# Optimization experiments

Hardware: AMD Instinct MI355X
Metric: run time of the kernel (lower is better)

The kernel has to match this reference:

```python
import jax, jax.numpy as jnp
import numpy as np

N_NODES = 50000
N_EDGES = 1500000
D = 512
LN_EPS = 1e-5


def setup_inputs() -> dict:
    key = jax.random.key(0)
    ks = jax.random.split(key, 8)
    scale = 1.0 / np.sqrt(D)
    return {
        "node_feature": jax.random.normal(ks[0], (N_NODES, D), dtype=jnp.float32),
        "edge_index": jax.random.randint(ks[1], (2, N_EDGES), 0, N_NODES, dtype=jnp.int32),
        "W_l": jax.random.uniform(ks[2], (D, D), jnp.float32, -scale, scale),  # neighbor lin
        "b_l": jnp.zeros((D,), jnp.float32),
        "W_r": jax.random.uniform(ks[3], (D, D), jnp.float32, -scale, scale),  # root lin (no bias)
        "gamma": jnp.ones((D,), jnp.float32),
        "beta": jnp.zeros((D,), jnp.float32),
    }


def _layer_norm(x, gamma, beta):
    mu = jnp.mean(x, axis=-1, keepdims=True)
    var = jnp.mean(jnp.square(x - mu), axis=-1, keepdims=True)
    return (x - mu) * jax.lax.rsqrt(var + LN_EPS) * gamma + beta


def reference(node_feature, edge_index, W_l, b_l, W_r, gamma, beta):
    n = node_feature.shape[0]
    residual = node_feature
    h = _layer_norm(node_feature, gamma, beta)
    src, dst = edge_index[0], edge_index[1]
    # mean-aggregate source features at destinations (gather + segment scatter)
    summed = jax.ops.segment_sum(h[src], dst, num_segments=n)  # [N, D]
    cnt = jax.ops.segment_sum(jnp.ones((src.shape[0],), h.dtype), dst, num_segments=n)
    mean = summed / jnp.maximum(cnt, 1.0)[:, None]
    # SAGEConv: lin_l(aggregated) + lin_r(root); bias on lin_l
    out = mean @ W_l.T + b_l + h @ W_r.T
    out = jax.nn.relu(out)
    return out + residual
```

## Files before the change

kernel.cpp:

```cpp
#include <hip/hip_runtime.h>


#define D_DIM 512

typedef __bf16 bf16x8 __attribute__((ext_vector_type(8)));
typedef float f32x4 __attribute__((ext_vector_type(4)));
typedef float f32x2 __attribute__((ext_vector_type(2)));

__device__ __forceinline__ unsigned short f2bf(float f) {
  unsigned u = __float_as_uint(f);
  u += 0x7fffu + ((u >> 16) & 1u);
  return (unsigned short)(u >> 16);
}
__device__ __forceinline__ float bflo(unsigned u) { return __uint_as_float(u << 16); }
__device__ __forceinline__ float bfhi(unsigned u) { return __uint_as_float(u & 0xffff0000u); }
__device__ __forceinline__ unsigned packbf2(float lo, float hi) {
  return (unsigned)f2bf(lo) | ((unsigned)f2bf(hi) << 16);
}

__global__ void ln_kernel(const float* __restrict__ x, const float* __restrict__ gamma,
                          const float* __restrict__ beta, unsigned short* __restrict__ Acat,
                          unsigned char* __restrict__ h8, int n, int use_fp8) {
  int lane = threadIdx.x & 63;
  int row = blockIdx.x * 4 + (threadIdx.x >> 6);
  if (row >= n) return;
  const float* xr = x + (size_t)row * D_DIM + lane * 8;
  float4 a = *(const float4*)xr;
  float4 b = *(const float4*)(xr + 4);
  float sum = a.x + a.y + a.z + a.w + b.x + b.y + b.z + b.w;
  float sq = a.x * a.x + a.y * a.y + a.z * a.z + a.w * a.w +
             b.x * b.x + b.y * b.y + b.z * b.z + b.w * b.w;
#pragma unroll
  for (int m = 1; m < 64; m <<= 1) {
    sum += __shfl_xor(sum, m, 64);
    sq  += __shfl_xor(sq, m, 64);
  }
  float mu = sum * (1.0f / D_DIM);
  float var = sq * (1.0f / D_DIM) - mu * mu;
  float rs = rsqrtf(var + 1e-5f);
  const float* gp = gamma + lane * 8;
  const float* bp = beta + lane * 8;
  float4 g0 = *(const float4*)gp, g1 = *(const float4*)(gp + 4);
  float4 e0 = *(const float4*)bp, e1 = *(const float4*)(bp + 4);
  float h0 = (a.x - mu) * rs * g0.x + e0.x;
  float h1 = (a.y - mu) * rs * g0.y + e0.y;
  float h2 = (a.z - mu) * rs * g0.z + e0.z;
  float h3 = (a.w - mu) * rs * g0.w + e0.w;
  float h4 = (b.x - mu) * rs * g1.x + e1.x;
  float h5 = (b.y - mu) * rs * g1.y + e1.y;
  float h6 = (b.z - mu) * rs * g1.z + e1.z;
  float h7 = (b.w - mu) * rs * g1.w + e1.w;
  uint4 st = { packbf2(h0, h1), packbf2(h2, h3), packbf2(h4, h5), packbf2(h6, h7) };
  *(uint4*)(Acat + (size_t)row * 1024 + 512 + lane * 8) = st;
  if (use_fp8) {
    int p0 = __builtin_amdgcn_cvt_pk_fp8_f32(h0, h1, 0, false);
    p0 = __builtin_amdgcn_cvt_pk_fp8_f32(h2, h3, p0, true);
    int p1 = __builtin_amdgcn_cvt_pk_fp8_f32(h4, h5, 0, false);
    p1 = __builtin_amdgcn_cvt_pk_fp8_f32(h6, h7, p1, true);
    uint2 st2 = { (unsigned)p0, (unsigned)p1 };
    *(uint2*)(h8 + (size_t)row * 512 + lane * 8) = st2;
  }
}

__global__ void wconv_kernel(const float* __restrict__ Wl, const float* __restrict__ Wr,
                             unsigned short* __restrict__ Wcat) {
  int id = blockIdx.x * 256 + threadIdx.x;
  int j = id >> 9, k = id & 511;
  Wcat[(size_t)j * 1024 + k] = f2bf(Wl[id]);
  Wcat[(size_t)j * 1024 + 512 + k] = f2bf(Wr[id]);
}

__global__ void zero_kernel(int* __restrict__ p, int n) {
  int i = blockIdx.x * 256 + threadIdx.x;
  if (i < n) p[i] = 0;
}

__global__ void hist_kernel(const int* __restrict__ dst, int nE, int* __restrict__ cnt) {
  int e = blockIdx.x * 256 + threadIdx.x;
  if (e < nE) atomicAdd(&cnt[dst[e]], 1);
}

__global__ void scan1_kernel(const int* __restrict__ cnt, int n,
                             int* __restrict__ excl, int* __restrict__ bsums) {
  __shared__ int wsum[16];
  int gid = blockIdx.x * 1024 + threadIdx.x;
  int lane = threadIdx.x & 63, wave = threadIdx.x >> 6;
  int v = (gid < n) ? cnt[gid] : 0;
  int s = v;
#pragma unroll
  for (int d = 1; d < 64; d <<= 1) {
    int t = __shfl_up(s, d, 64);
    if (lane >= d) s += t;
  }
  if (lane == 63) wsum[wave] = s;
  __syncthreads();
  if (wave == 0) {
    int ws = (lane < 16) ? wsum[lane] : 0;
#pragma unroll
    for (int d = 1; d < 16; d <<= 1) {
      int t = __shfl_up(ws, d, 64);
      if (lane >= d) ws += t;
    }
    if (lane < 16) wsum[lane] = ws;
  }
  __syncthreads();
  int incl = s + ((wave > 0) ? wsum[wave - 1] : 0);
  if (gid < n) excl[gid] = incl - v;
  if (threadIdx.x == 1023) bsums[blockIdx.x] = incl;
}

__global__ void scan2_kernel(int* __restrict__ bsums, int nb) {
  int lane = threadIdx.x;
  int v = (lane < nb) ? bsums[lane] : 0;
  int s = v;
#pragma unroll
  for (int d = 1; d < 64; d <<= 1) {
    int t = __shfl_up(s, d, 64);
    if (lane >= d) s += t;
  }
  if (lane < nb) bsums[lane] = s - v;
}

__global__ void scan3_kernel(int* __restrict__ rowst, int* __restrict__ cur,
                             const int* __restrict__ bsums, int n, int nE) {
  int gid = blockIdx.x * 1024 + threadIdx.x;
  if (gid < n) {
    int r = rowst[gid] + bsums[blockIdx.x];
    rowst[gid] = r;
    cur[gid] = r;
  }
  if (gid == 0) rowst[n] = nE;
}

__global__ void scatter_kernel(const int* __restrict__ src, const int* __restrict__ dst,
                               int nE, int* __restrict__ cur, int* __restrict__ sorted_src) {
  int e = blockIdx.x * 256 + threadIdx.x;
  if (e < nE) {
    int p = atomicAdd(&cur[dst[e]], 1);
    sorted_src[p] = src[e];
  }
}

__device__ __forceinline__ void acc_bf(float* acc, uint4 r) {
  acc[0] += bflo(r.x); acc[1] += bfhi(r.x);
  acc[2] += bflo(r.y); acc[3] += bfhi(r.y);
  acc[4] += bflo(r.z); acc[5] += bfhi(r.z);
  acc[6] += bflo(r.w); acc[7] += bfhi(r.w);
}

__device__ __forceinline__ void acc_f8(float* acc, uint2 r) {
  f32x2 a = __builtin_amdgcn_cvt_pk_f32_fp8(r.x, false);
  f32x2 b = __builtin_amdgcn_cvt_pk_f32_fp8(r.x, true);
  f32x2 c = __builtin_amdgcn_cvt_pk_f32_fp8(r.y, false);
  f32x2 d = __builtin_amdgcn_cvt_pk_f32_fp8(r.y, true);
  acc[0] += a.x; acc[1] += a.y; acc[2] += b.x; acc[3] += b.y;
  acc[4] += c.x; acc[5] += c.y; acc[6] += d.x; acc[7] += d.y;
}

__global__ void agg_kernel(unsigned short* __restrict__ Acat,
                           const unsigned char* __restrict__ h8,
                           const int* __restrict__ rowst,
                           const int* __restrict__ sorted_src, int n, int use_fp8) {
  int lane = threadIdx.x & 63;
  int node = blockIdx.x * 4 + (threadIdx.x >> 6);
  if (node >= n) return;
  int s0 = rowst[node], s1 = rowst[node + 1];
  float acc[8] = {0.f, 0.f, 0.f, 0.f, 0.f, 0.f, 0.f, 0.f};
  if (use_fp8) {
    const unsigned char* hb = h8 + lane * 8;
    int e = s0;
    for (; e + 3 < s1; e += 4) {
      int i0 = sorted_src[e], i1 = sorted_src[e + 1];
      int i2 = sorted_src[e + 2], i3 = sorted_src[e + 3];
      uint2 r0 = *(const uint2*)(hb + (size_t)i0 * 512);
      uint2 r1 = *(const uint2*)(hb + (size_t)i1 * 512);
      uint2 r2 = *(const uint2*)(hb + (size_t)i2 * 512);
      uint2 r3 = *(const uint2*)(hb + (size_t)i3 * 512);
      acc_f8(acc, r0); acc_f8(acc, r1); acc_f8(acc, r2); acc_f8(acc, r3);
    }
    for (; e < s1; ++e) {
      uint2 r0 = *(const uint2*)(hb + (size_t)sorted_src[e] * 512);
      acc_f8(acc, r0);
    }
  } else {
    const unsigned short* hbase = Acat + 512 + lane * 8;
    int e = s0;
    for (; e + 3 < s1; e += 4) {
      int i0 = sorted_src[e], i1 = sorted_src[e + 1];
      int i2 = sorted_src[e + 2], i3 = sorted_src[e + 3];
      uint4 r0 = *(const uint4*)(hbase + (size_t)i0 * 1024);
      uint4 r1 = *(const uint4*)(hbase + (size_t)i1 * 1024);
      uint4 r2 = *(const uint4*)(hbase + (size_t)i2 * 1024);
      uint4 r3 = *(const uint4*)(hbase + (size_t)i3 * 1024);
      acc_bf(acc, r0); acc_bf(acc, r1); acc_bf(acc, r2); acc_bf(acc, r3);
    }
    for (; e < s1; ++e) {
      uint4 r0 = *(const uint4*)(hbase + (size_t)sorted_src[e] * 1024);
      acc_bf(acc, r0);
    }
  }
  int deg = s1 - s0;
  float sc = (deg > 0) ? (1.0f / (float)deg) : 0.0f;
  uint4 st = { packbf2(acc[0] * sc, acc[1] * sc), packbf2(acc[2] * sc, acc[3] * sc),
               packbf2(acc[4] * sc, acc[5] * sc), packbf2(acc[6] * sc, acc[7] * sc) };
  *(uint4*)(Acat + (size_t)node * 1024 + lane * 8) = st;
}

__device__ __forceinline__ void async16(const unsigned short* g, char* lds) {
  __builtin_amdgcn_global_load_lds((const __attribute__((address_space(1))) void*)g,
                                   (__attribute__((address_space(3))) void*)lds, 16, 0, 0);
}

__global__ __launch_bounds__(256) void gemm_kernel(
    const unsigned short* __restrict__ A,
    const unsigned short* __restrict__ B,
    const float* __restrict__ bias,
    const float* __restrict__ residual,
    float* __restrict__ out, int M) {
  __shared__ unsigned short sA[128 * 32];
  __shared__ unsigned short sB[128 * 32];
  const int K = 1024;
  int t = threadIdx.x;
  int lane = t & 63, wave = t >> 6;
  int quad = lane >> 4, l16 = lane & 15;
  int mb = blockIdx.x >> 2, nb = blockIdx.x & 3;
  int mBase = mb * 128, nBase = nb * 128;
  int wm = (wave & 1) * 64, wn = (wave >> 1) * 64;

  const unsigned short* gA = A + (size_t)(mBase + (t >> 2)) * K + (t & 3) * 8;
  const unsigned short* gB = B + (size_t)(nBase + (t >> 2)) * K + (t & 3) * 8;
  char* lA0 = (char*)sA + wave * 1024;
  char* lA1 = (char*)sA + 4096 + wave * 1024;
  char* lB0 = (char*)sB + wave * 1024;
  char* lB1 = (char*)sB + 4096 + wave * 1024;

  f32x4 acc[4][4] = {};

  for (int ks = 0; ks < K; ks += 32) {
    __syncthreads();
    async16(gA + ks, lA0);
    async16(gA + (size_t)64 * K + ks, lA1);
    async16(gB + ks, lB0);
    async16(gB + (size_t)64 * K + ks, lB1);
    __syncthreads();
    bf16x8 af[4], bf[4];
#pragma unroll
    for (int i = 0; i < 4; ++i)
      af[i] = *(const bf16x8*)(sA + (wm + i * 16 + l16) * 32 + quad * 8);
#pragma unroll
    for (int j = 0; j < 4; ++j)
      bf[j] = *(const bf16x8*)(sB + (wn + j * 16 + l16) * 32 + quad * 8);
#pragma unroll
    for (int i = 0; i < 4; ++i)
#pragma unroll
      for (int j = 0; j < 4; ++j)
        acc[i][j] = __builtin_amdgcn_mfma_f32_16x16x32_bf16(af[i], bf[j], acc[i][j], 0, 0, 0);
  }

  float biasv[4];
#pragma unroll
  for (int j = 0; j < 4; ++j) biasv[j] = bias[nBase + wn + j * 16 + l16];
#pragma unroll
  for (int i = 0; i < 4; ++i) {
    int gr0 = mBase + wm + i * 16 + quad * 4;
#pragma unroll
    for (int j = 0; j < 4; ++j) {
      int col = nBase + wn + j * 16 + l16;
#pragma unroll
      for (int r = 0; r < 4; ++r) {
        int gr = gr0 + r;
        if (gr < M) {
          size_t idx = (size_t)gr * D_DIM + col;
          float v = acc[i][j][r] + biasv[j];
          float rv = __builtin_nontemporal_load(&residual[idx]);
          __builtin_nontemporal_store(fmaxf(v, 0.0f) + rv, &out[idx]);
        }
      }
    }
  }
}

extern "C" void kernel_launch(void* const* d_in, const int* in_sizes, int n_in,
                              void* d_out, int out_size, void* d_ws, size_t ws_size,
                              hipStream_t stream) {
  const float* x = (const float*)d_in[0];
  const int* ei = (const int*)d_in[1];
  const float* Wl = (const float*)d_in[2];
  const float* bl = (const float*)d_in[3];
  const float* Wr = (const float*)d_in[4];
  const float* gamma = (const float*)d_in[5];
  const float* beta = (const float*)d_in[6];
  float* out = (float*)d_out;

  int n = in_sizes[0] / D_DIM;
  int nE = in_sizes[1] / 2;
  const int* src = ei;
  const int* dstv = ei + nE;
  int Mpad = (n + 127) & ~127;

  char* w = (char*)d_ws;
  size_t off = 0;
  auto carve = [&](size_t bytes) {
    char* p = w + off;
    off += (bytes + 255) & ~(size_t)255;
    return p;
  };
  unsigned short* Acat = (unsigned short*)carve((size_t)Mpad * 1024 * 2);
  unsigned short* Wcat = (unsigned short*)carve((size_t)512 * 1024 * 2);
  int* sorted = (int*)carve((size_t)nE * 4);
  int* cnt = (int*)carve((size_t)n * 4);
  int* rowst = (int*)carve((size_t)(n + 1) * 4);
  int* bsums = (int*)carve(1024);
  if (off > ws_size) return;

  size_t h8_bytes = (size_t)n * 512;
  int use_fp8 = (off + h8_bytes <= ws_size) ? 1 : 0;
  unsigned char* h8 = use_fp8 ? (unsigned char*)carve(h8_bytes) : (unsigned char*)w;

  int nbScan = (n + 1023) / 1024;

  ln_kernel<<<(n + 3) / 4, 256, 0, stream>>>(x, gamma, beta, Acat, h8, n, use_fp8);
  wconv_kernel<<<(512 * 512) / 256, 256, 0, stream>>>(Wl, Wr, Wcat);
  zero_kernel<<<(n + 255) / 256, 256, 0, stream>>>(cnt, n);
  hist_kernel<<<(nE + 255) / 256, 256, 0, stream>>>(dstv, nE, cnt);
  scan1_kernel<<<nbScan, 1024, 0, stream>>>(cnt, n, rowst, bsums);
  scan2_kernel<<<1, 64, 0, stream>>>(bsums, nbScan);
  scan3_kernel<<<nbScan, 1024, 0, stream>>>(rowst, cnt, bsums, n, nE);
  scatter_kernel<<<(nE + 255) / 256, 256, 0, stream>>>(src, dstv, nE, cnt, sorted);
  agg_kernel<<<(n + 3) / 4, 256, 0, stream>>>(Acat, h8, rowst, sorted, n, use_fp8);
  gemm_kernel<<<(Mpad / 128) * 4, 256, 0, stream>>>(Acat, Wcat, bl, x, out, n);
}
```

Before: 652.3 us.

## Double-buffer GEMM LDS tiles and remap block order for L2 locality

The GEMM main loop now uses two LDS buffers, issuing the next K-slice's async global-to-LDS loads before computing the current one, with a vmcnt wait and a barrier in place of two full syncs per step. Block indices are also remapped so groups of 8 M-tiles share the same N-tile sequence, which is meant to improve L2 reuse of A and B. The cost is double the LDS footprint and a few wasted blocks that exit early from the padded grid.

```diff
diff --git a/kernel.cpp b/kernel.cpp
--- a/kernel.cpp
+++ b/kernel.cpp
@@ -216,46 +216,60 @@
     const unsigned short* __restrict__ B,
     const float* __restrict__ bias,
     const float* __restrict__ residual,
-    float* __restrict__ out, int M) {
-  __shared__ unsigned short sA[128 * 32];
-  __shared__ unsigned short sB[128 * 32];
+    float* __restrict__ out, int M, int Mblocks) {
+  __shared__ unsigned short sA[2][4096];
+  __shared__ unsigned short sB[2][4096];
   const int K = 1024;
   int t = threadIdx.x;
   int lane = t & 63, wave = t >> 6;
   int quad = lane >> 4, l16 = lane & 15;
-  int mb = blockIdx.x >> 2, nb = blockIdx.x & 3;
+  int b = blockIdx.x;
+  int mb = (b >> 5) * 8 + (b & 7);
+  int nb = (b >> 3) & 3;
+  if (mb >= Mblocks) return;
   int mBase = mb * 128, nBase = nb * 128;
   int wm = (wave & 1) * 64, wn = (wave >> 1) * 64;
 
   const unsigned short* gA = A + (size_t)(mBase + (t >> 2)) * K + (t & 3) * 8;
   const unsigned short* gB = B + (size_t)(nBase + (t >> 2)) * K + (t & 3) * 8;
-  char* lA0 = (char*)sA + wave * 1024;
-  char* lA1 = (char*)sA + 4096 + wave * 1024;
-  char* lB0 = (char*)sB + wave * 1024;
-  char* lB1 = (char*)sB + 4096 + wave * 1024;
 
   f32x4 acc[4][4] = {};
 
-  for (int ks = 0; ks < K; ks += 32) {
-    __syncthreads();
-    async16(gA + ks, lA0);
-    async16(gA + (size_t)64 * K + ks, lA1);
-    async16(gB + ks, lB0);
-    async16(gB + (size_t)64 * K + ks, lB1);
-    __syncthreads();
-    bf16x8 af[4], bf[4];
+  auto issue = [&](int ks, int buf) {
+    char* a0 = (char*)&sA[buf][0] + wave * 1024;
+    char* b0 = (char*)&sB[buf][0] + wave * 1024;
+    async16(gA + ks, a0);
+    async16(gA + (size_t)64 * K + ks, a0 + 4096);
+    async16(gB + ks, b0);
+    async16(gB + (size_t)64 * K + ks, b0 + 4096);
+  };
+  auto compute = [&](int buf) {
+    const unsigned short* pA = &sA[buf][0];
+    const unsigned short* pB = &sB[buf][0];
+    bf16x8 af[4], bfr[4];
 #pragma unroll
     for (int i = 0; i < 4; ++i)
-      af[i] = *(const bf16x8*)(sA + (wm + i * 16 + l16) * 32 + quad * 8);
+      af[i] = *(const bf16x8*)(pA + (wm + i * 16 + l16) * 32 + quad * 8);
 #pragma unroll
     for (int j = 0; j < 4; ++j)
-      bf[j] = *(const bf16x8*)(sB + (wn + j * 16 + l16) * 32 + quad * 8);
+      bfr[j] = *(const bf16x8*)(pB + (wn + j * 16 + l16) * 32 + quad * 8);
 #pragma unroll
     for (int i = 0; i < 4; ++i)
 #pragma unroll
       for (int j = 0; j < 4; ++j)
-        acc[i][j] = __builtin_amdgcn_mfma_f32_16x16x32_bf16(af[i], bf[j], acc[i][j], 0, 0, 0);
-  }
+        acc[i][j] = __builtin_amdgcn_mfma_f32_16x16x32_bf16(af[i], bfr[j], acc[i][j], 0, 0, 0);
+  };
+
+  issue(0, 0);
+  for (int r = 0; r < 31; ++r) {
+    int cur = r & 1;
+    issue((r + 1) << 5, cur ^ 1);
+    asm volatile("s_waitcnt vmcnt(4)\n\ts_barrier" ::: "memory");
+    compute(cur);
+    asm volatile("s_barrier" ::: "memory");
+  }
+  asm volatile("s_waitcnt vmcnt(0)\n\ts_barrier" ::: "memory");
+  compute(1);
 
   float biasv[4];
 #pragma unroll
@@ -297,6 +311,7 @@
   const int* src = ei;
   const int* dstv = ei + nE;
   int Mpad = (n + 127) & ~127;
+  int Mblocks = Mpad / 128;
 
   char* w = (char*)d_ws;
   size_t off = 0;
@@ -328,5 +343,6 @@
   scan3_kernel<<<nbScan, 1024, 0, stream>>>(rowst, cnt, bsums, n, nE);
   scatter_kernel<<<(nE + 255) / 256, 256, 0, stream>>>(src, dstv, nE, cnt, sorted);
   agg_kernel<<<(n + 3) / 4, 256, 0, stream>>>(Acat, h8, rowst, sorted, n, use_fp8);
-  gemm_kernel<<<(Mpad / 128) * 4, 256, 0, stream>>>(Acat, Wcat, bl, x, out, n);
-}
+  int gemmBlocks = ((Mblocks + 7) / 8) * 32;
+  gemm_kernel<<<gemmBlocks, 256, 0, stream>>>(Acat, Wcat, bl, x, out, n, Mblocks);
+}
```

Measured after the change: 647.6 us. Within noise of the previous version (-0.7%).
